# Optimization experiments

Measured on AMD Instinct MI355X. Metric: run time of the kernel, lower is better.

The kernel has to match this reference:

```python
import jax, jax.numpy as jnp
import numpy as np

BETA = 0.95
THR = 1.0
NUM_STEPS = 100
ALPHA = 2.0  # snntorch atan surrogate default

@jax.custom_vjp
def atan_spike(x):
    return (x > 0).astype(x.dtype)

def _as_fwd(x):
    return (x > 0).astype(x.dtype), x

def _as_bwd(x, g):
    return (g * (ALPHA / 2) / (1 + (jnp.pi / 2 * ALPHA * x) ** 2),)

atan_spike.defvjp(_as_fwd, _as_bwd)


def setup_inputs() -> dict:
    key = jax.random.key(0)
    ks = jax.random.split(key, 9)
    B = 16384
    SH, NH, CO, OUT = 1024, 1024, 256, 64
    s = 0.05
    return {
        "x": jax.random.normal(ks[0], (B, 105), jnp.float32),
        "snn_w1": jax.random.normal(ks[1], (SH, 5), jnp.float32) * s,
        "snn_b1": jnp.zeros((SH,), jnp.float32),
        "snn_w2": jax.random.normal(ks[2], (OUT, SH), jnp.float32) * s,
        "snn_b2": jnp.zeros((OUT,), jnp.float32),
        "nn_w1": jax.random.normal(ks[3], (NH, 5), jnp.float32) * s,
        "nn_b1": jnp.zeros((NH,), jnp.float32),
        "nn_w2": jax.random.normal(ks[4], (OUT, NH), jnp.float32) * s,
        "nn_b2": jnp.zeros((OUT,), jnp.float32),
        "conv_w": jax.random.normal(ks[5], (32, 1, 3), jnp.float32) * s,
        "conv_b": jnp.zeros((32,), jnp.float32),
        "cnn_fc_w": jax.random.normal(ks[6], (CO, 32 * 50), jnp.float32) * s,
        "cnn_fc_b": jnp.zeros((CO,), jnp.float32),
        "comb_w": jax.random.normal(ks[7], (OUT, 2 * OUT + CO), jnp.float32) * s,
        "comb_b": jnp.zeros((OUT,), jnp.float32),
    }


def _forward(x, snn_w1, snn_b1, snn_w2, snn_b2, nn_w1, nn_b1, nn_w2, nn_b2,
             conv_w, conv_b, cnn_fc_w, cnn_fc_b, comb_w, comb_b):
    feats = x[:, :5]                 # [B,5]
    wave = x[:, 5:][:, None, :]      # [B,1,100]
    B = x.shape[0]

    # ---- SNN branch (LIF, beta leak, subtract reset, threshold 1.0) ----
    cur1 = feats @ snn_w1.T + snn_b1  # input current is constant across steps

    def step(carry, _):
        mem1, spk1, mem2, spk2 = carry
        # reset term uses detached spike (snntorch mem_reset detaches)
        mem1 = BETA * mem1 + cur1 - jax.lax.stop_gradient(spk1) * THR
        spk1 = atan_spike(mem1 - THR)
        cur2 = spk1 @ snn_w2.T + snn_b2
        mem2 = BETA * mem2 + cur2 - jax.lax.stop_gradient(spk2) * THR
        spk2 = atan_spike(mem2 - THR)
        return (mem1, spk1, mem2, spk2), spk2

    z1 = jnp.zeros_like(cur1)
    z2 = jnp.zeros((B, snn_w2.shape[0]), cur1.dtype)
    _, spk_rec = jax.lax.scan(step, (z1, z1, z2, z2), None, length=NUM_STEPS)
    snn_out = spk_rec.mean(axis=0)   # [B,OUT]

    # ---- MLP branch ----
    nn_out = jax.nn.relu(feats @ nn_w1.T + nn_b1) @ nn_w2.T + nn_b2

    # ---- CNN branch ----
    c = jax.lax.conv_general_dilated(wave, conv_w, (1,), [(1, 1)],
                                     dimension_numbers=("NCW", "OIW", "NCW"))
    c = jax.nn.relu(c + conv_b[None, :, None])   # [B,32,100]
    c = c.reshape(B, 32, 50, 2).max(axis=-1)      # MaxPool1d(k=2,s=2)
    cnn_out = c.reshape(B, -1) @ cnn_fc_w.T + cnn_fc_b

    combined = jnp.concatenate([snn_out, nn_out, cnn_out], axis=1)
    return combined @ comb_w.T + comb_b


def reference(x, snn_w1, snn_b1, snn_w2, snn_b2, nn_w1, nn_b1, nn_w2, nn_b2,
              conv_w, conv_b, cnn_fc_w, cnn_fc_b, comb_w, comb_b):
    return _forward(x, snn_w1, snn_b1, snn_w2, snn_b2, nn_w1, nn_b1, nn_w2,
                    nn_b2, conv_w, conv_b, cnn_fc_w, cnn_fc_b, comb_w, comb_b)
```

## Files before the change

### kernel.cpp

```cpp
#include <hip/hip_runtime.h>

typedef __bf16 bf16x8_t __attribute__((ext_vector_type(8)));
typedef float f32x4_t __attribute__((ext_vector_type(4)));
typedef float f32x2_t __attribute__((ext_vector_type(2)));

#define NSTEPS 100
#define COMBF 51200u

static __device__ __forceinline__ unsigned short f2bfu(float v) {
  union { __bf16 h; unsigned short u; } c; c.h = (__bf16)v; return c.u;
}
static __device__ __forceinline__ unsigned int pack2bf(float a, float b) {
  return (unsigned)f2bfu(a) | ((unsigned)f2bfu(b) << 16);
}
union BF8U { unsigned int u[4]; bf16x8_t v; };

static __device__ __forceinline__ void pk_mul_ip(f32x2_t &a, f32x2_t b) {
  asm("v_pk_mul_f32 %0, %0, %1" : "+v"(a) : "v"(b));
}
static __device__ __forceinline__ void pk_add_ip(f32x2_t &a, f32x2_t b) {
  asm("v_pk_add_f32 %0, %0, %1" : "+v"(a) : "v"(b));
}

static __device__ __forceinline__ bf16x8_t bfrag_f32(const float* __restrict__ p, float s) {
  BF8U r;
#pragma unroll
  for (int i = 0; i < 4; ++i) r.u[i] = pack2bf(p[2*i]*s, p[2*i+1]*s);
  return r.v;
}

static __device__ __forceinline__ void comb_store(unsigned char* ldsp, int k, int row, float v) {
  *(unsigned short*)(ldsp + COMBF +
      (unsigned)((k >> 5)*1024 + (((k >> 3) & 3)*16 + row)*16 + (k & 7)*2)) = f2bfu(v);
}

__global__ __launch_bounds__(512, 2)
void hybrid_v7(const float* __restrict__ x,
               const float* __restrict__ snn_w1, const float* __restrict__ snn_b1,
               const float* __restrict__ snn_w2, const float* __restrict__ snn_b2,
               const float* __restrict__ nn_w1,  const float* __restrict__ nn_b1,
               const float* __restrict__ nn_w2,  const float* __restrict__ nn_b2,
               const float* __restrict__ conv_w, const float* __restrict__ conv_b,
               const float* __restrict__ fc_w,   const float* __restrict__ fc_b,
               const float* __restrict__ comb_w, const float* __restrict__ comb_b,
               const unsigned short* __restrict__ fcwb, int use_bf,
               float* __restrict__ out)
{
  __shared__ __align__(16) unsigned char lds[131072];
  const int tid  = threadIdx.x;
  const int w    = tid >> 6;
  const int l    = tid & 63;
  const int q    = l >> 4;
  const int m    = l & 15;
  const int row0 = blockIdx.x * 16;

  const int hi  = w >> 2;
  const int ntr = w & 3;
  const int rn  = ntr*16 + m;
  const int rA  = hi*4 + q;

  const float* xr = x + (row0 + m)*105;
  const float f0 = xr[0], f1 = xr[1], f2 = xr[2], f3 = xr[3], f4 = xr[4];
  const float b2l = snn_b2[rn];

  bf16x8_t bfr[4][4];
#pragma unroll
  for (int ci = 0; ci < 4; ++ci)
#pragma unroll
    for (int nt = 0; nt < 4; ++nt)
      bfr[ci][nt] = bfrag_f32(snn_w2 + (nt*16 + m)*1024 + (w*4 + ci)*32 + q*8, 1.f);

  f32x2_t c2[16], mem2[16], spneg2[16];
  f32x2_t beta2; beta2.x = 0.95f; beta2.y = 0.95f;
  {
    const int kb = w*128 + q*8;
#pragma unroll
    for (int ci = 0; ci < 4; ++ci) {
      const float* wp = snn_w1 + (kb + ci*32)*5;
      float wa[40];
#pragma unroll
      for (int u2 = 0; u2 < 10; ++u2) {
        const float4 t4 = *(const float4*)(wp + u2*4);
        wa[u2*4+0] = t4.x; wa[u2*4+1] = t4.y; wa[u2*4+2] = t4.z; wa[u2*4+3] = t4.w;
      }
      float cc[8];
#pragma unroll
      for (int j = 0; j < 8; ++j)
        cc[j] = f0*wa[j*5] + f1*wa[j*5+1] + f2*wa[j*5+2] + f3*wa[j*5+3] + f4*wa[j*5+4]
              + snn_b1[kb + ci*32 + j];
#pragma unroll
      for (int jj = 0; jj < 4; ++jj) {
        f32x2_t t; t.x = cc[2*jj]; t.y = cc[2*jj+1];
        c2[ci*4+jj] = t;
        f32x2_t z; z.x = 0.f; z.y = 0.f;
        mem2[ci*4+jj] = z;
        f32x2_t nz; nz.x = -0.0f; nz.y = -0.0f;
        spneg2[ci*4+jj] = nz;
      }
    }
  }

  BF8U afr[4];
  auto lif_step = [&]() {
#pragma unroll
    for (int i = 0; i < 16; ++i) {
      pk_mul_ip(mem2[i], beta2);
      pk_add_ip(mem2[i], c2[i]);
      pk_add_ip(mem2[i], spneg2[i]);
      f32x2_t sn;
      sn.x = mem2[i].x > 1.f ? -1.0f : -0.0f;
      sn.y = mem2[i].y > 1.f ? -1.0f : -0.0f;
      spneg2[i] = sn;
      afr[i>>2].u[i&3] =
          __builtin_amdgcn_perm(__float_as_uint(sn.y), __float_as_uint(sn.x), 0x07060302u)
          & 0x3F803F80u;
    }
  };
  lif_step();

  f32x2_t m2;     m2.x = 0.f;      m2.y = 0.f;
  f32x2_t s2neg;  s2neg.x = -0.0f; s2neg.y = -0.0f;
  f32x2_t cntneg; cntneg.x = 0.f;  cntneg.y = 0.f;
  f32x2_t sbias2; sbias2.x = b2l;  sbias2.y = b2l;

  const unsigned wbase = (unsigned)(w*4096 + (q&1)*2048 + (q>>1)*4 + m*8);
  const unsigned rbase = (unsigned)(rA*512 + rn*8);
  const f32x4_t z4 = {0.f, 0.f, 0.f, 0.f};

  auto reduce_lif2 = [&](f32x2_t v[8]) {
    pk_add_ip(v[0], v[1]); pk_add_ip(v[2], v[3]);
    pk_add_ip(v[4], v[5]); pk_add_ip(v[6], v[7]);
    pk_add_ip(v[0], v[2]); pk_add_ip(v[4], v[6]);
    pk_add_ip(v[0], v[4]);
    pk_add_ip(v[0], sbias2);
    pk_mul_ip(m2, beta2);
    pk_add_ip(m2, v[0]);
    pk_add_ip(m2, s2neg);
    s2neg.x = m2.x > 1.f ? -1.0f : -0.0f;
    s2neg.y = m2.y > 1.f ? -1.0f : -0.0f;
    pk_add_ip(cntneg, s2neg);
  };

#pragma unroll 1
  for (int ss = 0; ss < 25; ++ss) {
#pragma unroll 1
    for (int k = 0; k < 4; ++k) {
      f32x4_t acc[4] = {z4, z4, z4, z4};
#pragma unroll
      for (int ci = 0; ci < 4; ++ci)
#pragma unroll
        for (int nt = 0; nt < 4; ++nt)
          acc[nt] = __builtin_amdgcn_mfma_f32_16x16x32_bf16(afr[ci].v, bfr[ci][nt], acc[nt], 0,0,0);
      if (ss*4 + k < NSTEPS - 1) lif_step();
      unsigned char* wp = lds + (unsigned)(k*32768) + wbase;
#pragma unroll
      for (int nt = 0; nt < 4; ++nt)
#pragma unroll
        for (int r = 0; r < 4; ++r)
          *(float*)(wp + (unsigned)(r*512 + nt*128)) = acc[nt][r];
    }
    __syncthreads();

    {
      const unsigned char* rp = lds + rbase;
      f32x2_t va[8], vb[8];
#pragma unroll
      for (int s = 0; s < 8; ++s) va[s] = *(const f32x2_t*)(rp + (unsigned)(s*4096));
#pragma unroll
      for (int s = 0; s < 8; ++s) vb[s] = *(const f32x2_t*)(rp + 32768u + (unsigned)(s*4096));
      reduce_lif2(va);
      reduce_lif2(vb);
#pragma unroll
      for (int s = 0; s < 8; ++s) va[s] = *(const f32x2_t*)(rp + 65536u + (unsigned)(s*4096));
#pragma unroll
      for (int s = 0; s < 8; ++s) vb[s] = *(const f32x2_t*)(rp + 98304u + (unsigned)(s*4096));
      reduce_lif2(va);
      reduce_lif2(vb);
    }
    __syncthreads();
  }

#pragma unroll
  for (int ci = 0; ci < 4; ++ci)
#pragma unroll
    for (int nt = 0; nt < 4; ++nt)
      bfr[ci][nt] = bfrag_f32(nn_w2 + (nt*16 + m)*1024 + (w*4 + ci)*32 + q*8, 1.f);
  {
    BF8U hfr[4];
    const int kb = w*128 + q*8;
#pragma unroll
    for (int ci = 0; ci < 4; ++ci) {
      const float* wp = nn_w1 + (kb + ci*32)*5;
      float wa[40];
#pragma unroll
      for (int u2 = 0; u2 < 10; ++u2) {
        const float4 t4 = *(const float4*)(wp + u2*4);
        wa[u2*4+0] = t4.x; wa[u2*4+1] = t4.y; wa[u2*4+2] = t4.z; wa[u2*4+3] = t4.w;
      }
      float hv[8];
#pragma unroll
      for (int j = 0; j < 8; ++j) {
        const float h = f0*wa[j*5] + f1*wa[j*5+1] + f2*wa[j*5+2] + f3*wa[j*5+3] + f4*wa[j*5+4]
                      + nn_b1[kb + ci*32 + j];
        hv[j] = fmaxf(h, 0.f);
      }
#pragma unroll
      for (int jj = 0; jj < 4; ++jj) hfr[ci].u[jj] = pack2bf(hv[2*jj], hv[2*jj+1]);
    }
    f32x4_t acc[4] = {z4, z4, z4, z4};
#pragma unroll
    for (int ci = 0; ci < 4; ++ci)
#pragma unroll
      for (int nt = 0; nt < 4; ++nt)
        acc[nt] = __builtin_amdgcn_mfma_f32_16x16x32_bf16(hfr[ci].v, bfr[ci][nt], acc[nt], 0,0,0);
#pragma unroll
    for (int nt = 0; nt < 4; ++nt)
#pragma unroll
      for (int r = 0; r < 4; ++r)
        *(float*)(lds + wbase + (unsigned)(r*512 + nt*128)) = acc[nt][r];
  }
  __syncthreads();
  {
    f32x2_t va[8];
    const unsigned char* rp = lds + rbase;
#pragma unroll
    for (int s = 0; s < 8; ++s) va[s] = *(const f32x2_t*)(rp + (unsigned)(s*4096));
    pk_add_ip(va[0], va[1]); pk_add_ip(va[2], va[3]);
    pk_add_ip(va[4], va[5]); pk_add_ip(va[6], va[7]);
    pk_add_ip(va[0], va[2]); pk_add_ip(va[4], va[6]);
    pk_add_ip(va[0], va[4]);
    const float nb = nn_b2[rn];
    f32x2_t nb2; nb2.x = nb; nb2.y = nb;
    pk_add_ip(va[0], nb2);
    comb_store(lds, rn,      rA,     cntneg.x * -0.0078125f);
    comb_store(lds, rn,      rA + 8, cntneg.y * -0.0078125f);
    comb_store(lds, 64 + rn, rA,     va[0].x);
    comb_store(lds, 64 + rn, rA + 8, va[0].y);
  }
  __syncthreads();

  {
    const int ch = tid >> 4;
    const float cw0 = conv_w[ch*3+0], cw1 = conv_w[ch*3+1], cw2 = conv_w[ch*3+2];
    const float cbb = conv_b[ch];
    const float* xw = xr + 5;
    float xm1 = 0.f, x0v = xw[0];
#pragma unroll 1
    for (int p = 0; p < 50; ++p) {
      const float xp1 = xw[2*p + 1];
      const float xp2 = (p < 49) ? xw[2*p + 2] : 0.f;
      const float av = cw0*xm1 + cw1*x0v + cw2*xp1 + cbb;
      const float bv = cw0*x0v + cw1*xp1 + cw2*xp2 + cbb;
      const float pv = fmaxf(fmaxf(av, 0.f), fmaxf(bv, 0.f));
      const int k = ch*50 + p;
      *(unsigned short*)(lds + (unsigned)((k>>5)*1024 + (((k>>3)&3)*16 + m)*16 + (k&7)*2)) = f2bfu(pv);
      xm1 = xp1; x0v = xp2;
    }
  }
  __syncthreads();

  {
    const int c0 = (w*2 + 0)*16 + m;
    const int c1 = (w*2 + 1)*16 + m;
    f32x4_t e0 = z4, o0 = z4, e1 = z4, o1 = z4;
    if (use_bf) {
#pragma unroll 2
      for (int kc = 0; kc < 50; kc += 2) {
        const bf16x8_t a0 = *(const bf16x8_t*)(lds + (unsigned)((kc*64 + l)*16));
        const bf16x8_t a1 = *(const bf16x8_t*)(lds + (unsigned)(((kc+1)*64 + l)*16));
        e0 = __builtin_amdgcn_mfma_f32_16x16x32_bf16(a0, *(const bf16x8_t*)(fcwb + c0*1600 + kc*32 + q*8), e0, 0,0,0);
        o0 = __builtin_amdgcn_mfma_f32_16x16x32_bf16(a1, *(const bf16x8_t*)(fcwb + c0*1600 + (kc+1)*32 + q*8), o0, 0,0,0);
        e1 = __builtin_amdgcn_mfma_f32_16x16x32_bf16(a0, *(const bf16x8_t*)(fcwb + c1*1600 + kc*32 + q*8), e1, 0,0,0);
        o1 = __builtin_amdgcn_mfma_f32_16x16x32_bf16(a1, *(const bf16x8_t*)(fcwb + c1*1600 + (kc+1)*32 + q*8), o1, 0,0,0);
      }
    } else {
#pragma unroll 2
      for (int kc = 0; kc < 50; kc += 2) {
        const bf16x8_t a0 = *(const bf16x8_t*)(lds + (unsigned)((kc*64 + l)*16));
        const bf16x8_t a1 = *(const bf16x8_t*)(lds + (unsigned)(((kc+1)*64 + l)*16));
        e0 = __builtin_amdgcn_mfma_f32_16x16x32_bf16(a0, bfrag_f32(fc_w + c0*1600 + kc*32 + q*8, 1.f), e0, 0,0,0);
        o0 = __builtin_amdgcn_mfma_f32_16x16x32_bf16(a1, bfrag_f32(fc_w + c0*1600 + (kc+1)*32 + q*8, 1.f), o0, 0,0,0);
        e1 = __builtin_amdgcn_mfma_f32_16x16x32_bf16(a0, bfrag_f32(fc_w + c1*1600 + kc*32 + q*8, 1.f), e1, 0,0,0);
        o1 = __builtin_amdgcn_mfma_f32_16x16x32_bf16(a1, bfrag_f32(fc_w + c1*1600 + (kc+1)*32 + q*8, 1.f), o1, 0,0,0);
      }
    }
    const float fb0 = fc_b[c0], fb1 = fc_b[c1];
#pragma unroll
    for (int r = 0; r < 4; ++r) {
      comb_store(lds, 128 + c0, q*4 + r, (e0[r] + o0[r]) + fb0);
      comb_store(lds, 128 + c1, q*4 + r, (e1[r] + o1[r]) + fb1);
    }
  }
  __syncthreads();

  if (w < 4) {
    const int cn = w*16 + m;
    f32x4_t oe = z4, oo = z4;
#pragma unroll
    for (int kc = 0; kc < 12; kc += 2) {
      const bf16x8_t a0 = *(const bf16x8_t*)(lds + COMBF + (unsigned)((kc*64 + l)*16));
      const bf16x8_t a1 = *(const bf16x8_t*)(lds + COMBF + (unsigned)(((kc+1)*64 + l)*16));
      const float s0 = (kc    < 2) ? 1.28f : 1.f;
      const float s1 = (kc+1 < 2) ? 1.28f : 1.f;
      oe = __builtin_amdgcn_mfma_f32_16x16x32_bf16(a0, bfrag_f32(comb_w + cn*384 + kc*32 + q*8, s0), oe, 0,0,0);
      oo = __builtin_amdgcn_mfma_f32_16x16x32_bf16(a1, bfrag_f32(comb_w + cn*384 + (kc+1)*32 + q*8, s1), oo, 0,0,0);
    }
    const float cb2 = comb_b[cn];
#pragma unroll
    for (int r = 0; r < 4; ++r)
      out[(row0 + q*4 + r)*64 + cn] = (oe[r] + oo[r]) + cb2;
  }
}

__global__ __launch_bounds__(256)
void fcw_to_bf16(const float* __restrict__ src, unsigned short* __restrict__ dst) {
  const int i = (blockIdx.x * 256 + threadIdx.x) * 4;
  const float4 v = *(const float4*)(src + i);
  ushort4 o;
  o.x = f2bfu(v.x); o.y = f2bfu(v.y); o.z = f2bfu(v.z); o.w = f2bfu(v.w);
  *(ushort4*)(dst + i) = o;
}

extern "C" void kernel_launch(void* const* d_in, const int* in_sizes, int n_in,
                              void* d_out, int out_size, void* d_ws, size_t ws_size,
                              hipStream_t stream) {
  const float* x       = (const float*)d_in[0];
  const float* snn_w1  = (const float*)d_in[1];
  const float* snn_b1  = (const float*)d_in[2];
  const float* snn_w2  = (const float*)d_in[3];
  const float* snn_b2  = (const float*)d_in[4];
  const float* nn_w1   = (const float*)d_in[5];
  const float* nn_b1   = (const float*)d_in[6];
  const float* nn_w2   = (const float*)d_in[7];
  const float* nn_b2   = (const float*)d_in[8];
  const float* conv_w  = (const float*)d_in[9];
  const float* conv_b  = (const float*)d_in[10];
  const float* fc_w    = (const float*)d_in[11];
  const float* fc_b    = (const float*)d_in[12];
  const float* comb_w  = (const float*)d_in[13];
  const float* comb_b  = (const float*)d_in[14];
  float* outp = (float*)d_out;

  const int rows = in_sizes[0] / 105;
  const int grid = rows / 16;

  const size_t fcw_elems = (size_t)in_sizes[11];
  const int use_bf = (ws_size >= fcw_elems * 2) ? 1 : 0;
  unsigned short* fcwb = (unsigned short*)d_ws;
  if (use_bf) {
    fcw_to_bf16<<<dim3((unsigned)(fcw_elems / 1024)), dim3(256), 0, stream>>>(fc_w, fcwb);
  }

  hybrid_v7<<<dim3(grid), dim3(512), 0, stream>>>(
      x, snn_w1, snn_b1, snn_w2, snn_b2,
      nn_w1, nn_b1, nn_w2, nn_b2,
      conv_w, conv_b, fc_w, fc_b, comb_w, comb_b,
      fcwb, use_bf, outp);
}
```

Baseline: 700.8 us.

## Double-buffer LIF layer-2 partial sums with one barrier per step

Replaces the four-step batched LDS staging (128 KB, two barriers per four steps) with a ping-pong pair of 32 KB buffers. Each step writes its MFMA partials to one buffer and reduces the previous step's partials from the other, with a single __syncthreads per step. The partial stores now use inline-asm ds_write2_b32. LDS use halves, which could allow more resident blocks per CU, but there are now four barriers per four steps instead of two.

```diff
diff --git a/kernel.cpp b/kernel.cpp
--- a/kernel.cpp
+++ b/kernel.cpp
@@ -5,6 +5,8 @@
 typedef float f32x2_t __attribute__((ext_vector_type(2)));
 
 #define NSTEPS 100
+#define PB0 0u
+#define PB1 32768u
 #define COMBF 51200u
 
 static __device__ __forceinline__ unsigned short f2bfu(float v) {
@@ -35,18 +37,18 @@
 }
 
 __global__ __launch_bounds__(512, 2)
-void hybrid_v7(const float* __restrict__ x,
-               const float* __restrict__ snn_w1, const float* __restrict__ snn_b1,
-               const float* __restrict__ snn_w2, const float* __restrict__ snn_b2,
-               const float* __restrict__ nn_w1,  const float* __restrict__ nn_b1,
-               const float* __restrict__ nn_w2,  const float* __restrict__ nn_b2,
-               const float* __restrict__ conv_w, const float* __restrict__ conv_b,
-               const float* __restrict__ fc_w,   const float* __restrict__ fc_b,
-               const float* __restrict__ comb_w, const float* __restrict__ comb_b,
-               const unsigned short* __restrict__ fcwb, int use_bf,
-               float* __restrict__ out)
+void hybrid_v12(const float* __restrict__ x,
+                const float* __restrict__ snn_w1, const float* __restrict__ snn_b1,
+                const float* __restrict__ snn_w2, const float* __restrict__ snn_b2,
+                const float* __restrict__ nn_w1,  const float* __restrict__ nn_b1,
+                const float* __restrict__ nn_w2,  const float* __restrict__ nn_b2,
+                const float* __restrict__ conv_w, const float* __restrict__ conv_b,
+                const float* __restrict__ fc_w,   const float* __restrict__ fc_b,
+                const float* __restrict__ comb_w, const float* __restrict__ comb_b,
+                const unsigned short* __restrict__ fcwb, int use_bf,
+                float* __restrict__ out)
 {
-  __shared__ __align__(16) unsigned char lds[131072];
+  __shared__ __align__(16) unsigned char lds[65536];
   const int tid  = threadIdx.x;
   const int w    = tid >> 6;
   const int l    = tid & 63;
@@ -127,7 +129,16 @@
   const unsigned rbase = (unsigned)(rA*512 + rn*8);
   const f32x4_t z4 = {0.f, 0.f, 0.f, 0.f};
 
-  auto reduce_lif2 = [&](f32x2_t v[8]) {
+  const unsigned a0_pb0 = (unsigned)(uintptr_t)(lds + PB0 + wbase);
+  const unsigned a1_pb0 = a0_pb0 + 1024u;
+  const unsigned a0_pb1 = (unsigned)(uintptr_t)(lds + PB1 + wbase);
+  const unsigned a1_pb1 = a0_pb1 + 1024u;
+
+  auto reduce_lif2 = [&](unsigned prv) {
+    const unsigned char* rp = lds + prv + rbase;
+    f32x2_t v[8];
+#pragma unroll
+    for (int s = 0; s < 8; ++s) v[s] = *(const f32x2_t*)(rp + (unsigned)(s*4096));
     pk_add_ip(v[0], v[1]); pk_add_ip(v[2], v[3]);
     pk_add_ip(v[4], v[5]); pk_add_ip(v[6], v[7]);
     pk_add_ip(v[0], v[2]); pk_add_ip(v[4], v[6]);
@@ -141,43 +152,40 @@
     pk_add_ip(cntneg, s2neg);
   };
 
+  auto phase = [&](unsigned wa0, unsigned wa1, unsigned prv, bool doRead, bool doLif) {
+    f32x4_t acc[4] = {z4, z4, z4, z4};
+#pragma unroll
+    for (int ci = 0; ci < 4; ++ci)
+#pragma unroll
+      for (int nt = 0; nt < 4; ++nt)
+        acc[nt] = __builtin_amdgcn_mfma_f32_16x16x32_bf16(afr[ci].v, bfr[ci][nt], acc[nt], 0,0,0);
+    if (doLif) lif_step();
+    asm volatile(
+      "ds_write2_b32 %0, %2, %3 offset0:0  offset1:128\n\t"
+      "ds_write2_b32 %1, %4, %5 offset0:0  offset1:128\n\t"
+      "ds_write2_b32 %0, %6, %7 offset0:32 offset1:160\n\t"
+      "ds_write2_b32 %1, %8, %9 offset0:32 offset1:160"
+      :: "v"(wa0), "v"(wa1),
+         "v"(acc[0][0]), "v"(acc[0][1]), "v"(acc[0][2]), "v"(acc[0][3]),
+         "v"(acc[1][0]), "v"(acc[1][1]), "v"(acc[1][2]), "v"(acc[1][3])
+      : "memory");
+    asm volatile(
+      "ds_write2_b32 %0, %2, %3 offset0:64 offset1:192\n\t"
+      "ds_write2_b32 %1, %4, %5 offset0:64 offset1:192\n\t"
+      "ds_write2_b32 %0, %6, %7 offset0:96 offset1:224\n\t"
+      "ds_write2_b32 %1, %8, %9 offset0:96 offset1:224"
+      :: "v"(wa0), "v"(wa1),
+         "v"(acc[2][0]), "v"(acc[2][1]), "v"(acc[2][2]), "v"(acc[2][3]),
+         "v"(acc[3][0]), "v"(acc[3][1]), "v"(acc[3][2]), "v"(acc[3][3])
+      : "memory");
+    if (doRead) reduce_lif2(prv);
+    __syncthreads();
+  };
+
 #pragma unroll 1
-  for (int ss = 0; ss < 25; ++ss) {
-#pragma unroll 1
-    for (int k = 0; k < 4; ++k) {
-      f32x4_t acc[4] = {z4, z4, z4, z4};
-#pragma unroll
-      for (int ci = 0; ci < 4; ++ci)
-#pragma unroll
-        for (int nt = 0; nt < 4; ++nt)
-          acc[nt] = __builtin_amdgcn_mfma_f32_16x16x32_bf16(afr[ci].v, bfr[ci][nt], acc[nt], 0,0,0);
-      if (ss*4 + k < NSTEPS - 1) lif_step();
-      unsigned char* wp = lds + (unsigned)(k*32768) + wbase;
-#pragma unroll
-      for (int nt = 0; nt < 4; ++nt)
-#pragma unroll
-        for (int r = 0; r < 4; ++r)
-          *(float*)(wp + (unsigned)(r*512 + nt*128)) = acc[nt][r];
-    }
-    __syncthreads();
-
-    {
-      const unsigned char* rp = lds + rbase;
-      f32x2_t va[8], vb[8];
-#pragma unroll
-      for (int s = 0; s < 8; ++s) va[s] = *(const f32x2_t*)(rp + (unsigned)(s*4096));
-#pragma unroll
-      for (int s = 0; s < 8; ++s) vb[s] = *(const f32x2_t*)(rp + 32768u + (unsigned)(s*4096));
-      reduce_lif2(va);
-      reduce_lif2(vb);
-#pragma unroll
-      for (int s = 0; s < 8; ++s) va[s] = *(const f32x2_t*)(rp + 65536u + (unsigned)(s*4096));
-#pragma unroll
-      for (int s = 0; s < 8; ++s) vb[s] = *(const f32x2_t*)(rp + 98304u + (unsigned)(s*4096));
-      reduce_lif2(va);
-      reduce_lif2(vb);
-    }
-    __syncthreads();
+  for (int tt = 0; tt < NSTEPS; tt += 2) {
+    phase(a0_pb0, a1_pb0, PB1, tt > 0, true);
+    phase(a0_pb1, a1_pb1, PB0, true,  tt + 1 < NSTEPS - 1);
   }
 
 #pragma unroll
@@ -186,6 +194,8 @@
     for (int nt = 0; nt < 4; ++nt)
       bfr[ci][nt] = bfrag_f32(nn_w2 + (nt*16 + m)*1024 + (w*4 + ci)*32 + q*8, 1.f);
   {
+    reduce_lif2(PB1);
+
     BF8U hfr[4];
     const int kb = w*128 + q*8;
 #pragma unroll
@@ -217,25 +227,25 @@
     for (int nt = 0; nt < 4; ++nt)
 #pragma unroll
       for (int r = 0; r < 4; ++r)
-        *(float*)(lds + wbase + (unsigned)(r*512 + nt*128)) = acc[nt][r];
+        *(float*)(lds + PB0 + wbase + (unsigned)(r*512 + nt*128)) = acc[nt][r];
   }
   __syncthreads();
   {
-    f32x2_t va[8];
-    const unsigned char* rp = lds + rbase;
-#pragma unroll
-    for (int s = 0; s < 8; ++s) va[s] = *(const f32x2_t*)(rp + (unsigned)(s*4096));
-    pk_add_ip(va[0], va[1]); pk_add_ip(va[2], va[3]);
-    pk_add_ip(va[4], va[5]); pk_add_ip(va[6], va[7]);
-    pk_add_ip(va[0], va[2]); pk_add_ip(va[4], va[6]);
-    pk_add_ip(va[0], va[4]);
+    f32x2_t v[8];
+    const unsigned char* rp = lds + PB0 + rbase;
+#pragma unroll
+    for (int s = 0; s < 8; ++s) v[s] = *(const f32x2_t*)(rp + (unsigned)(s*4096));
+    pk_add_ip(v[0], v[1]); pk_add_ip(v[2], v[3]);
+    pk_add_ip(v[4], v[5]); pk_add_ip(v[6], v[7]);
+    pk_add_ip(v[0], v[2]); pk_add_ip(v[4], v[6]);
+    pk_add_ip(v[0], v[4]);
     const float nb = nn_b2[rn];
     f32x2_t nb2; nb2.x = nb; nb2.y = nb;
-    pk_add_ip(va[0], nb2);
+    pk_add_ip(v[0], nb2);
     comb_store(lds, rn,      rA,     cntneg.x * -0.0078125f);
     comb_store(lds, rn,      rA + 8, cntneg.y * -0.0078125f);
-    comb_store(lds, 64 + rn, rA,     va[0].x);
-    comb_store(lds, 64 + rn, rA + 8, va[0].y);
+    comb_store(lds, 64 + rn, rA,     v[0].x);
+    comb_store(lds, 64 + rn, rA + 8, v[0].y);
   }
   __syncthreads();
 
@@ -351,7 +361,7 @@
     fcw_to_bf16<<<dim3((unsigned)(fcw_elems / 1024)), dim3(256), 0, stream>>>(fc_w, fcwb);
   }
 
-  hybrid_v7<<<dim3(grid), dim3(512), 0, stream>>>(
+  hybrid_v12<<<dim3(grid), dim3(512), 0, stream>>>(
       x, snn_w1, snn_b1, snn_w2, snn_b2,
       nn_w1, nn_b1, nn_w2, nn_b2,
       conv_w, conv_b, fc_w, fc_b, comb_w, comb_b,
```

Measured after the change: 746.7 us. 6.5% more time.
